# Kernel optimization log

Hardware: AMD Instinct MI355X
Metric: run time of the kernel (lower is better)

Reference implementation:

```python
import jax, jax.numpy as jnp
import numpy as np

EPS = 1e-8  # matches torch F.cosine_similarity default eps


def setup_inputs() -> dict:
    key = jax.random.key(0)
    kq, km = jax.random.split(key)
    B, M, D = 4096, 65536, 512
    return {
        "query_features": jax.random.normal(kq, (B, D), dtype=jnp.float32),
        "memory": jax.random.normal(km, (M, D), dtype=jnp.float32),
        "k": 8,
    }


def reference(query_features, memory, k):
    # cosine similarity: normalize rows (clamped norm like torch eps), then GEMM
    qn = query_features / jnp.maximum(
        jnp.linalg.norm(query_features, axis=-1, keepdims=True), EPS)
    mn = memory / jnp.maximum(
        jnp.linalg.norm(memory, axis=-1, keepdims=True), EPS)
    sims = jnp.einsum("bd,md->bm", qn, mn)          # [B, M]
    _, top_idx = jax.lax.top_k(sims, k)              # [B, k]
    # gather memory rows and average over the k neighbors
    return memory[top_idx].mean(axis=1)              # [B, D]
```

## Files before the change

kernel.cpp:

```cpp
#include <hip/hip_runtime.h>
#include <hip/hip_bf16.h>

#define B_ROWS 4096
#define M_ROWS 65536
#define DIM 512
#define TOPK 8
#define CAP 512
#define NR 16
#define TAU 0.132583f
#define FB_N 2048

typedef unsigned short u16;
typedef unsigned int u32;
typedef signed char s8;
typedef unsigned char u8;
typedef int i32x4 __attribute__((ext_vector_type(4)));

__device__ inline void gl_lds16(const void* g, void* l) {
  __builtin_amdgcn_global_load_lds(
      (const __attribute__((address_space(1))) u32*)g,
      (__attribute__((address_space(3))) u32*)l, 16, 0, 0);
}

__global__ __launch_bounds__(256) void quant_kernel(const float* __restrict__ mem,
                                                    const float* __restrict__ q,
                                                    s8* __restrict__ mn8,
                                                    s8* __restrict__ qn8,
                                                    float* __restrict__ sb,
                                                    float* __restrict__ sa) {
  int gw = (int)((blockIdx.x * 256 + threadIdx.x) >> 6);
  int lane = threadIdx.x & 63;
  const float* in;
  s8* out;
  float* scale;
  int row;
  if (gw < M_ROWS) {
    in = mem; out = mn8; scale = sb; row = gw;
  } else {
    in = q; out = qn8; scale = sa; row = gw - M_ROWS;
  }
  const float4* r = (const float4*)(in + (size_t)row * DIM);
  float4 v0 = r[lane * 2 + 0];
  float4 v1 = r[lane * 2 + 1];
  float ss = v0.x*v0.x + v0.y*v0.y + v0.z*v0.z + v0.w*v0.w
           + v1.x*v1.x + v1.y*v1.y + v1.z*v1.z + v1.w*v1.w;
#pragma unroll
  for (int off = 32; off > 0; off >>= 1) ss += __shfl_xor(ss, off);
  float inv = 1.0f / fmaxf(sqrtf(ss), 1e-8f);
  float x[8] = {v0.x*inv, v0.y*inv, v0.z*inv, v0.w*inv,
                v1.x*inv, v1.y*inv, v1.z*inv, v1.w*inv};
  float ma = 0.f;
#pragma unroll
  for (int e = 0; e < 8; e++) ma = fmaxf(ma, fabsf(x[e]));
#pragma unroll
  for (int off = 32; off > 0; off >>= 1) ma = fmaxf(ma, __shfl_xor(ma, off));
  float s = fmaxf(ma, 1e-20f) * (1.0f / 127.0f);
  float rs = 1.0f / s;
  u32 lo = 0, hi = 0;
#pragma unroll
  for (int e = 0; e < 4; e++) {
    int qi = __float2int_rn(fminf(fmaxf(x[e] * rs, -127.f), 127.f));
    lo |= ((u32)(u8)(s8)qi) << (8 * e);
  }
#pragma unroll
  for (int e = 0; e < 4; e++) {
    int qi = __float2int_rn(fminf(fmaxf(x[4 + e] * rs, -127.f), 127.f));
    hi |= ((u32)(u8)(s8)qi) << (8 * e);
  }
  uint2 pk; pk.x = lo; pk.y = hi;
  *(uint2*)(out + (size_t)row * DIM + lane * 8) = pk;
  if (lane == 0) scale[row] = s;
}

__global__ __launch_bounds__(256, 4) void gemm_select(const s8* __restrict__ qn,
                                                      const s8* __restrict__ mn,
                                                      const float* __restrict__ sa,
                                                      const float* __restrict__ sb,
                                                      int* __restrict__ count,
                                                      u32* __restrict__ cand) {
  __shared__ s8 sA[2][8192];
  __shared__ s8 sB[2][8192];

  int bid0 = blockIdx.x;
  int b1 = (bid0 & 7) * 2048 + (bid0 >> 3);
  int qtile = (b1 >> 12) * 8 + (b1 & 7);
  int mtile = (b1 >> 3) & 511;

  int tid = threadIdx.x;
  int lane = tid & 63;
  int w = tid >> 6;
  int wr = w >> 1, wc = w & 1;
  int rlo = lane & 15;
  int khi16 = (lane >> 4) << 4;

  const s8* gA = qn + (size_t)qtile * 128 * DIM;
  const s8* gB = mn + (size_t)mtile * 128 * DIM;

  int brow_lo = tid >> 3;
  int innb = (tid & 7) << 4;
  int inns = innb ^ ((brow_lo & 7) << 4);
  int grow0 = brow_lo * 2 + (inns >> 6);
  int gcolb = inns & 63;

  const s8* gA0 = gA + (size_t)grow0 * DIM + gcolb;
  const s8* gA1 = gA + (size_t)(grow0 + 64) * DIM + gcolb;
  const s8* gB0 = gB + (size_t)grow0 * DIM + gcolb;
  const s8* gB1 = gB + (size_t)(grow0 + 64) * DIM + gcolb;
  s8* lA0 = &sA[0][w * 1024];
  s8* lA1 = &sA[0][4096 + w * 1024];
  s8* lB0 = &sB[0][w * 1024];
  s8* lB1 = &sB[0][4096 + w * 1024];

  auto stage = [&](int slot, int kt) {
    int so = slot * 8192;
    gl_lds16(gA0 + kt * 64, lA0 + so);
    gl_lds16(gA1 + kt * 64, lA1 + so);
    gl_lds16(gB0 + kt * 64, lB0 + so);
    gl_lds16(gB1 + kt * 64, lB1 + so);
  };

  auto physof = [&](int row) {
    int brow = row >> 1;
    return (brow << 7) + ((((row & 1) << 6) + khi16) ^ ((brow & 7) << 4));
  };
  const char* rbA = (const char*)&sA[0][0];
  const char* rbB = (const char*)&sB[0][0];
  int offA[4], offB[4];
#pragma unroll
  for (int i = 0; i < 4; i++) {
    offA[i] = physof(wr * 64 + i * 16 + rlo);
    offB[i] = physof(wc * 64 + i * 16 + rlo);
  }

  i32x4 acc[4][4];
#pragma unroll
  for (int i = 0; i < 4; i++)
#pragma unroll
    for (int jj = 0; jj < 4; jj++) {
      i32x4 z = {0, 0, 0, 0};
      acc[i][jj] = z;
    }

  stage(0, 0);

#pragma unroll
  for (int t = 0; t < 8; t++) {
    asm volatile("s_waitcnt vmcnt(0)" ::: "memory");
    __builtin_amdgcn_s_barrier();
    const int cs = t & 1;
    if (t < 7) stage(cs ^ 1, t + 1);
    i32x4 aF[4], bF[4];
#pragma unroll
    for (int mi = 0; mi < 4; mi++) aF[mi] = *(const i32x4*)(rbA + cs * 8192 + offA[mi]);
#pragma unroll
    for (int ni = 0; ni < 4; ni++) bF[ni] = *(const i32x4*)(rbB + cs * 8192 + offB[ni]);
    __builtin_amdgcn_s_setprio(1);
#pragma unroll
    for (int mi = 0; mi < 4; mi++)
#pragma unroll
      for (int ni = 0; ni < 4; ni++)
        acc[mi][ni] = __builtin_amdgcn_mfma_i32_16x16x64_i8(aF[mi], bF[ni], acc[mi][ni], 0, 0, 0);
    __builtin_amdgcn_s_setprio(0);
  }

  int qbase = qtile * 128 + wr * 64 + (lane >> 4) * 4;
  int mbase = mtile * 128 + wc * 64 + (lane & 15);
#pragma unroll
  for (int mi = 0; mi < 4; mi++) {
    float4 sav = *(const float4*)&sa[qbase + mi * 16];
#pragma unroll
    for (int ni = 0; ni < 4; ni++) {
      float sbv = sb[mbase + ni * 16];
#pragma unroll
      for (int r = 0; r < 4; r++) {
        float v = (float)acc[mi][ni][r] * (sav[r] * sbv);
        if (v > TAU) {
          int qq = qbase + mi * 16 + r;
          u32 pk = (__builtin_bit_cast(u32, v) & 0xFFFF0000u) | (u32)(mbase + ni * 16);
          int pos = atomicAdd(&count[qq], 1);
          if (pos < CAP) cand[(size_t)qq * CAP + pos] = pk;
        }
      }
    }
  }
}

__global__ __launch_bounds__(256) void topk_kernel(const float* __restrict__ q,
                                                   const float* __restrict__ mem,
                                                   const int* __restrict__ count,
                                                   const u32* __restrict__ cand,
                                                   float* __restrict__ out) {
  __shared__ double s_sims[FB_N];
  __shared__ int s_cidx[FB_N];
  __shared__ double s_red[4];
  __shared__ int s_redj[4];
  __shared__ u32 s_pk[CAP];
  __shared__ int s_sel[NR];
  __shared__ double s_x[NR];
  __shared__ int s_win[TOPK];

  int b = blockIdx.x;
  int tid = threadIdx.x;
  int lane = tid & 63;
  int w = tid >> 6;

  const float* qrow = q + (size_t)b * DIM;
  const float4* qv = (const float4*)qrow;
  float4 q0 = qv[lane * 2], q1 = qv[lane * 2 + 1];
  double q8[8] = {q0.x, q0.y, q0.z, q0.w, q1.x, q1.y, q1.z, q1.w};
  double qq = 0;
#pragma unroll
  for (int e = 0; e < 8; e++) qq += q8[e] * q8[e];
#pragma unroll
  for (int off = 32; off > 0; off >>= 1) qq += __shfl_xor(qq, off);
  double qnorm = fmax(sqrt(qq), 1e-8);

  int c = count[b];
  if (c >= TOPK && c <= CAP) {
    for (int j = tid; j < c; j += 256) s_pk[j] = cand[(size_t)b * CAP + j];
    __syncthreads();
    int nsel = c < NR ? c : NR;
    if (w == 0) {
      for (int r = 0; r < nsel; r++) {
        int best = -1, bj = -1;
        for (int j = lane; j < c; j += 64) {
          int v = (int)s_pk[j];
          if (v > best) { best = v; bj = j; }
        }
#pragma unroll
        for (int off = 32; off > 0; off >>= 1) {
          int ov = __shfl_down(best, off);
          int oj = __shfl_down(bj, off);
          if (ov > best) { best = ov; bj = oj; }
        }
        bj = __shfl(bj, 0);
        if (lane == 0) { s_sel[r] = (int)(s_pk[bj] & 0xFFFFu); s_pk[bj] = 0; }
      }
    }
    __syncthreads();
    for (int i = w; i < nsel; i += 4) {
      int mi = s_sel[i];
      const float4* mv = (const float4*)(mem + (size_t)mi * DIM);
      float4 m0 = mv[lane * 2], m1 = mv[lane * 2 + 1];
      double m8[8] = {m0.x, m0.y, m0.z, m0.w, m1.x, m1.y, m1.z, m1.w};
      double dot = 0, mm = 0;
#pragma unroll
      for (int e = 0; e < 8; e++) { dot += q8[e] * m8[e]; mm += m8[e] * m8[e]; }
#pragma unroll
      for (int off = 32; off > 0; off >>= 1) {
        dot += __shfl_xor(dot, off);
        mm += __shfl_xor(mm, off);
      }
      if (lane == 0) s_x[i] = dot / (qnorm * fmax(sqrt(mm), 1e-8));
    }
    __syncthreads();
    if (w == 0) {
      double myv = (lane < nsel) ? s_x[lane] : -1e300;
      int myrow = (lane < nsel) ? s_sel[lane] : -1;
      for (int r = 0; r < TOPK; r++) {
        double bv = myv; int bl = lane;
#pragma unroll
        for (int off = 32; off > 0; off >>= 1) {
          double ov = __shfl_down(bv, off);
          int ol = __shfl_down(bl, off);
          if (ov > bv) { bv = ov; bl = ol; }
        }
        bl = __shfl(bl, 0);
        int brow = __shfl(myrow, bl);
        if (lane == 0) s_win[r] = brow;
        if (lane == bl) myv = -1e300;
      }
    }
    __syncthreads();
  } else {
    double tv[8]; int tix[8];
#pragma unroll
    for (int r = 0; r < 8; r++) { tv[r] = -1e300; tix[r] = -1; }
    for (int row = tid; row < M_ROWS; row += 256) {
      const float4* mv = (const float4*)(mem + (size_t)row * DIM);
      double dot = 0, mm = 0;
      for (int e = 0; e < DIM / 4; e++) {
        float4 m4 = mv[e], qk = qv[e];
        dot += (double)m4.x * qk.x + (double)m4.y * qk.y + (double)m4.z * qk.z + (double)m4.w * qk.w;
        mm  += (double)m4.x * m4.x + (double)m4.y * m4.y + (double)m4.z * m4.z + (double)m4.w * m4.w;
      }
      double sim = dot / (qnorm * fmax(sqrt(mm), 1e-8));
      int am = 0;
#pragma unroll
      for (int r = 1; r < 8; r++) if (tv[r] < tv[am]) am = r;
      if (sim > tv[am]) { tv[am] = sim; tix[am] = row; }
    }
#pragma unroll
    for (int r = 0; r < 8; r++) { s_sims[tid * 8 + r] = tv[r]; s_cidx[tid * 8 + r] = tix[r]; }
    __syncthreads();
    for (int r = 0; r < TOPK; r++) {
      double best = -1e300; int bj = -1;
      for (int j = tid; j < FB_N; j += 256) {
        double v = s_sims[j];
        if (v > best) { best = v; bj = j; }
      }
#pragma unroll
      for (int off = 32; off > 0; off >>= 1) {
        double ov = __shfl_down(best, off);
        int oj = __shfl_down(bj, off);
        if (ov > best) { best = ov; bj = oj; }
      }
      if (lane == 0) { s_red[w] = best; s_redj[w] = bj; }
      __syncthreads();
      if (tid == 0) {
        double bb = s_red[0]; int jj = s_redj[0];
        for (int i = 1; i < 4; i++) if (s_red[i] > bb) { bb = s_red[i]; jj = s_redj[i]; }
        s_win[r] = s_cidx[jj];
        s_sims[jj] = -1e300;
      }
      __syncthreads();
    }
  }

  float ax = 0.f, ay = 0.f;
#pragma unroll
  for (int r = 0; r < TOPK; r++) {
    const float2 v = *(const float2*)(mem + (size_t)s_win[r] * DIM + tid * 2);
    ax += v.x; ay += v.y;
  }
  float2 o; o.x = ax * 0.125f; o.y = ay * 0.125f;
  *(float2*)(out + (size_t)b * DIM + tid * 2) = o;
}

extern "C" void kernel_launch(void* const* d_in, const int* in_sizes, int n_in,
                              void* d_out, int out_size, void* d_ws, size_t ws_size,
                              hipStream_t stream) {
  (void)in_sizes; (void)n_in; (void)out_size; (void)ws_size;
  const float* q = (const float*)d_in[0];
  const float* mem = (const float*)d_in[1];
  float* out = (float*)d_out;

  char* ws = (char*)d_ws;
  s8* mn8 = (s8*)ws;
  s8* qn8 = (s8*)(ws + (size_t)M_ROWS * DIM);
  float* sb = (float*)(ws + (size_t)(M_ROWS + B_ROWS) * DIM);
  float* sa = (float*)((char*)sb + (size_t)M_ROWS * sizeof(float));
  int* count = (int*)((char*)sa + (size_t)B_ROWS * sizeof(float));
  u32* cand = (u32*)((char*)count + (size_t)B_ROWS * sizeof(int));

  hipMemsetAsync(count, 0, B_ROWS * sizeof(int), stream);
  quant_kernel<<<(M_ROWS + B_ROWS) / 4, 256, 0, stream>>>(mem, q, mn8, qn8, sb, sa);
  gemm_select<<<(B_ROWS / 128) * (M_ROWS / 128), 256, 0, stream>>>(qn8, mn8, sa, sb, count, cand);
  topk_kernel<<<B_ROWS, 256, 0, stream>>>(q, mem, count, cand, out);
}
```

Before: 305.7 us.

## Preload query A tile into registers and stage only memory tile via LDS

Each wave now loads its whole 64x512 int8 slice of the query tile straight from global memory into registers (32 i32x4 vectors) before the K loop, instead of staging A through shared memory each step. Only the memory (B) tile is still double-buffered through LDS. This halves LDS traffic and global-to-LDS staging per iteration. In exchange it costs about 128 extra VGPRs per thread, so launch bounds drop from 4 to 2 blocks per CU, which lowers occupancy. The A loads are also uncoalesced 16-byte row reads issued up front.

```diff
diff --git a/kernel.cpp b/kernel.cpp
--- a/kernel.cpp
+++ b/kernel.cpp
@@ -72,13 +72,12 @@
   if (lane == 0) scale[row] = s;
 }
 
-__global__ __launch_bounds__(256, 4) void gemm_select(const s8* __restrict__ qn,
+__global__ __launch_bounds__(256, 2) void gemm_select(const s8* __restrict__ qn,
                                                       const s8* __restrict__ mn,
                                                       const float* __restrict__ sa,
                                                       const float* __restrict__ sb,
                                                       int* __restrict__ count,
                                                       u32* __restrict__ cand) {
-  __shared__ s8 sA[2][8192];
   __shared__ s8 sB[2][8192];
 
   int bid0 = blockIdx.x;
@@ -93,7 +92,6 @@
   int rlo = lane & 15;
   int khi16 = (lane >> 4) << 4;
 
-  const s8* gA = qn + (size_t)qtile * 128 * DIM;
   const s8* gB = mn + (size_t)mtile * 128 * DIM;
 
   int brow_lo = tid >> 3;
@@ -102,35 +100,35 @@
   int grow0 = brow_lo * 2 + (inns >> 6);
   int gcolb = inns & 63;
 
-  const s8* gA0 = gA + (size_t)grow0 * DIM + gcolb;
-  const s8* gA1 = gA + (size_t)(grow0 + 64) * DIM + gcolb;
   const s8* gB0 = gB + (size_t)grow0 * DIM + gcolb;
   const s8* gB1 = gB + (size_t)(grow0 + 64) * DIM + gcolb;
-  s8* lA0 = &sA[0][w * 1024];
-  s8* lA1 = &sA[0][4096 + w * 1024];
   s8* lB0 = &sB[0][w * 1024];
   s8* lB1 = &sB[0][4096 + w * 1024];
 
-  auto stage = [&](int slot, int kt) {
+  auto stageB = [&](int slot, int kt) {
     int so = slot * 8192;
-    gl_lds16(gA0 + kt * 64, lA0 + so);
-    gl_lds16(gA1 + kt * 64, lA1 + so);
     gl_lds16(gB0 + kt * 64, lB0 + so);
     gl_lds16(gB1 + kt * 64, lB1 + so);
   };
+
+  i32x4 aA[8][4];
+  {
+    const s8* gAb = qn + (size_t)(qtile * 128 + wr * 64 + rlo) * DIM + khi16;
+#pragma unroll
+    for (int kt = 0; kt < 8; kt++)
+#pragma unroll
+      for (int mi = 0; mi < 4; mi++)
+        aA[kt][mi] = *(const i32x4*)(gAb + (size_t)mi * 16 * DIM + kt * 64);
+  }
 
   auto physof = [&](int row) {
     int brow = row >> 1;
     return (brow << 7) + ((((row & 1) << 6) + khi16) ^ ((brow & 7) << 4));
   };
-  const char* rbA = (const char*)&sA[0][0];
   const char* rbB = (const char*)&sB[0][0];
-  int offA[4], offB[4];
-#pragma unroll
-  for (int i = 0; i < 4; i++) {
-    offA[i] = physof(wr * 64 + i * 16 + rlo);
-    offB[i] = physof(wc * 64 + i * 16 + rlo);
-  }
+  int offB[4];
+#pragma unroll
+  for (int i = 0; i < 4; i++) offB[i] = physof(wc * 64 + i * 16 + rlo);
 
   i32x4 acc[4][4];
 #pragma unroll
@@ -141,17 +139,15 @@
       acc[i][jj] = z;
     }
 
-  stage(0, 0);
+  stageB(0, 0);
 
 #pragma unroll
   for (int t = 0; t < 8; t++) {
     asm volatile("s_waitcnt vmcnt(0)" ::: "memory");
     __builtin_amdgcn_s_barrier();
     const int cs = t & 1;
-    if (t < 7) stage(cs ^ 1, t + 1);
-    i32x4 aF[4], bF[4];
-#pragma unroll
-    for (int mi = 0; mi < 4; mi++) aF[mi] = *(const i32x4*)(rbA + cs * 8192 + offA[mi]);
+    if (t < 7) stageB(cs ^ 1, t + 1);
+    i32x4 bF[4];
 #pragma unroll
     for (int ni = 0; ni < 4; ni++) bF[ni] = *(const i32x4*)(rbB + cs * 8192 + offB[ni]);
     __builtin_amdgcn_s_setprio(1);
@@ -159,7 +155,7 @@
     for (int mi = 0; mi < 4; mi++)
 #pragma unroll
       for (int ni = 0; ni < 4; ni++)
-        acc[mi][ni] = __builtin_amdgcn_mfma_i32_16x16x64_i8(aF[mi], bF[ni], acc[mi][ni], 0, 0, 0);
+        acc[mi][ni] = __builtin_amdgcn_mfma_i32_16x16x64_i8(aA[t][mi], bF[ni], acc[mi][ni], 0, 0, 0);
     __builtin_amdgcn_s_setprio(0);
   }
 
```

New measurement: 547.4 us. +79.1%, slower.
